# Performance work log

Hardware: AMD Instinct MI355X
Metric: run time of the kernel (lower is better)

## Reference

```python
import jax, jax.numpy as jnp
import numpy as np

S = 256          # spatial coordinate range per axis
B = 2            # batch size
R = S + 2        # packing radix (padded so +-1 kernel offsets stay in range)
C = 64           # feature channels


def _pack(xyz, b):
    """Collision-free integer packing of (x,y,z,batch) -> int64 key.
    Faithful stand-in for torchsparse F.sphash (an injective hash of 4D coords)."""
    xyz = xyz.astype(jnp.int64) + 1  # shift so offset -1 maps to >= 0
    b = b.astype(jnp.int64)
    return ((b * R + xyz[:, 0]) * R + xyz[:, 1]) * R + xyz[:, 2]


def _offsets():
    # get_kernel_offsets(3, stride=input_stride=1, dilation=1): odd kernel -> z-major order
    r = np.arange(-1, 2)
    return np.array([[x, y, z] for z in r for y in r for x in r], dtype=np.int32)  # [27, 3]


def setup_inputs() -> dict:
    rng = np.random.default_rng(0)
    N0 = 1_200_000
    xyz = rng.integers(0, S, size=(N0, 3))
    bat = rng.integers(0, B, size=(N0, 1))
    coords = np.unique(np.concatenate([xyz, bat], axis=1), axis=0).astype(np.int32)  # [N,4]
    # spdownsample(coords, stride=2): floor to stride grid, unique rows
    dc = coords.copy()
    dc[:, :3] = dc[:, :3] // 2 * 2
    down_coords = np.unique(dc, axis=0).astype(np.int32)  # [M,4]
    key = jax.random.key(0)
    feats = jax.random.normal(key, (coords.shape[0], C), dtype=jnp.float32)
    return {
        "feats": feats,
        "coords": jnp.asarray(coords),
        "down_coords": jnp.asarray(down_coords),
    }


def reference(feats, coords, down_coords):
    N = feats.shape[0]
    # references = sphash(coords); build sorted key table for hash queries
    refs = _pack(coords[:, :3], coords[:, 3])
    order = jnp.argsort(refs)
    refs_sorted = refs[order]
    neg = jnp.asarray(-jnp.inf, feats.dtype)
    out = jnp.full((down_coords.shape[0], feats.shape[1]), neg, feats.dtype)
    # queries = sphash(down_coords, offsets); results = sphashquery; voxel_scatter_max
    # (output row of each nbmap entry is the query row, so scatter-max reduces to a
    #  per-row running maximum over the 27 fixed kernel offsets)
    for off in _offsets():
        q = _pack(down_coords[:, :3] + jnp.asarray(off), down_coords[:, 3])
        pos = jnp.clip(jnp.searchsorted(refs_sorted, q), 0, N - 1)
        match = refs_sorted[pos] == q            # [M] valid-neighbor mask (result != -1)
        src = order[pos]                          # [M] input voxel index per query
        out = jnp.maximum(out, jnp.where(match[:, None], feats[src], neg))
    # rows with no neighbor (cannot happen for stride-2 floor downsample) -> 0
    return jnp.where(jnp.isinf(out), jnp.asarray(0.0, feats.dtype), out)
```

## Files before the change

### kernel.cpp

```cpp
#include <hip/hip_runtime.h>
#include <cstdint>
#include <cstddef>

#define RADIX 258
#define EMPTY_ENTRY 0xFFFFFFFFFFFFFFFFULL
#define MAP_DIM 128
#define MAP_SLOTS (2 * MAP_DIM * MAP_DIM * MAP_DIM)

typedef float f32x4 __attribute__((ext_vector_type(4)));


__global__ __launch_bounds__(256) void build_map_kernel(
    const int* __restrict__ down, int M, unsigned* __restrict__ map)
{
    int j = blockIdx.x * blockDim.x + threadIdx.x;
    if (j >= M) return;
    const int4 c = ((const int4*)down)[j];
    unsigned idx = (((unsigned)(c.w * MAP_DIM + (c.x >> 1)) * MAP_DIM)
                    + (unsigned)(c.y >> 1)) * MAP_DIM + (unsigned)(c.z >> 1);
    map[idx] = (unsigned)j;
}

__global__ __launch_bounds__(256) void scatter_kernel(
    const int* __restrict__ coords, int N,
    const unsigned* __restrict__ map,
    unsigned* __restrict__ cnt, unsigned* __restrict__ nbmap)
{
    int i = blockIdx.x * blockDim.x + threadIdx.x;
    if (i >= N) return;
    const int4 c = ((const int4*)coords)[i];
    int qx[2], qy[2], qz[2];
    int nx = 1, ny = 1, nz = 1;
    if (c.x & 1) { qx[0] = (c.x - 1) >> 1; if (c.x + 1 <= 254) qx[nx++] = (c.x + 1) >> 1; }
    else         { qx[0] = c.x >> 1; }
    if (c.y & 1) { qy[0] = (c.y - 1) >> 1; if (c.y + 1 <= 254) qy[ny++] = (c.y + 1) >> 1; }
    else         { qy[0] = c.y >> 1; }
    if (c.z & 1) { qz[0] = (c.z - 1) >> 1; if (c.z + 1 <= 254) qz[nz++] = (c.z + 1) >> 1; }
    else         { qz[0] = c.z >> 1; }
    unsigned bbase = (unsigned)(c.w * MAP_DIM);
    for (int ix = 0; ix < nx; ++ix) {
        unsigned xb = (bbase + (unsigned)qx[ix]) * MAP_DIM;
        for (int iy = 0; iy < ny; ++iy) {
            unsigned yb = (xb + (unsigned)qy[iy]) * MAP_DIM;
            for (int iz = 0; iz < nz; ++iz) {
                unsigned qi = map[yb + (unsigned)qz[iz]];
                if (qi != 0xFFFFFFFFu) {
                    unsigned pos = atomicAdd(&cnt[qi], 1u);
                    nbmap[(size_t)qi * 27 + pos] = (unsigned)i;
                }
            }
        }
    }
}

__global__ __launch_bounds__(256) void gather4_kernel(
    const float* __restrict__ feats,
    const unsigned* __restrict__ cnt,
    const unsigned* __restrict__ nbmap,
    float* __restrict__ out, int M, int nwg)
{
    int bid = blockIdx.x;
    int q = nwg >> 3, r = nwg & 7;
    int xcd = bid & 7, orig = bid >> 3;
    int swz = (xcd < r ? xcd * (q + 1) : r * (q + 1) + (xcd - r) * q) + orig;

    int lane = threadIdx.x & 63;
    int g    = lane >> 4;
    int j    = lane & 15;
    int wave = swz * 4 + (int)(threadIdx.x >> 6);
    int row  = wave * 4 + g;
    bool valid = row < M;

    int c = valid ? (int)cnt[row] : 0;
    const unsigned* nb = nbmap + (size_t)row * 27;
    int idxA = 0;
    if (valid && j < c) idxA = (int)nb[j];

    const f32x4* f4 = (const f32x4*)feats;
    int gb = g << 4;
    f32x4 acc = {-INFINITY, -INFINITY, -INFINITY, -INFINITY};
    for (int r4 = 0; r4 < c; r4 += 4) {
        int cm1 = c - 1;
        int h0 = min(r4,     cm1);
        int h1 = min(r4 + 1, cm1);
        int h2 = min(r4 + 2, cm1);
        int h3 = min(r4 + 3, cm1);
        int a0 = __shfl(idxA, gb + min(h0, 15));
        int a1 = __shfl(idxA, gb + min(h1, 15));
        int a2 = __shfl(idxA, gb + min(h2, 15));
        int a3 = __shfl(idxA, gb + min(h3, 15));
        int s0 = (h0 < 16) ? a0 : (int)nb[h0];
        int s1 = (h1 < 16) ? a1 : (int)nb[h1];
        int s2 = (h2 < 16) ? a2 : (int)nb[h2];
        int s3 = (h3 < 16) ? a3 : (int)nb[h3];
        f32x4 v0 = f4[(size_t)s0 * 16 + j];
        f32x4 v1 = f4[(size_t)s1 * 16 + j];
        f32x4 v2 = f4[(size_t)s2 * 16 + j];
        f32x4 v3 = f4[(size_t)s3 * 16 + j];
        acc.x = fmaxf(fmaxf(fmaxf(acc.x, v0.x), fmaxf(v1.x, v2.x)), v3.x);
        acc.y = fmaxf(fmaxf(fmaxf(acc.y, v0.y), fmaxf(v1.y, v2.y)), v3.y);
        acc.z = fmaxf(fmaxf(fmaxf(acc.z, v0.z), fmaxf(v1.z, v2.z)), v3.z);
        acc.w = fmaxf(fmaxf(fmaxf(acc.w, v0.w), fmaxf(v1.w, v2.w)), v3.w);
    }
    if (valid) {
        if (c == 0) acc = (f32x4){0.f, 0.f, 0.f, 0.f};
        __builtin_nontemporal_store(acc, (f32x4*)out + (size_t)row * 16 + j);
    }
}


__global__ __launch_bounds__(256) void build_hash_kernel(
    const int* __restrict__ coords, int N,
    unsigned long long* __restrict__ tab, unsigned tmask, int tshift)
{
    int i = blockIdx.x * blockDim.x + threadIdx.x;
    if (i >= N) return;
    int x = coords[i * 4 + 0];
    int y = coords[i * 4 + 1];
    int z = coords[i * 4 + 2];
    int b = coords[i * 4 + 3];
    unsigned key = ((unsigned)(b * RADIX + x + 1) * RADIX + (unsigned)(y + 1)) * RADIX
                   + (unsigned)(z + 1);
    unsigned long long entry = ((unsigned long long)key << 32) | (unsigned)i;
    unsigned slot = (key * 2654435761u) >> tshift;
    while (true) {
        unsigned long long prev = atomicCAS(&tab[slot], EMPTY_ENTRY, entry);
        if (prev == EMPTY_ENTRY) break;
        slot = (slot + 1) & tmask;
    }
}

__global__ __launch_bounds__(256) void pool_kernel(
    const float* __restrict__ feats,
    const int* __restrict__ down, int M,
    const unsigned long long* __restrict__ tab, unsigned tmask, int tshift,
    float* __restrict__ out)
{
    int wave = (int)((blockIdx.x * blockDim.x + threadIdx.x) >> 6);
    int lane = threadIdx.x & 63;
    if (wave >= M) return;

    const int* dc = down + (size_t)wave * 4;
    int dx = dc[0], dy = dc[1], dz = dc[2], db = dc[3];
    unsigned base = ((unsigned)(db * RADIX + dx + 1) * RADIX + (unsigned)(dy + 1)) * RADIX
                    + (unsigned)(dz + 1);

    int src = -1;
    if (lane < 27) {
        int ox = lane % 3 - 1;
        int oy = (lane / 3) % 3 - 1;
        int oz = lane / 9 - 1;
        int delta = ox * (RADIX * RADIX) + oy * RADIX + oz;
        unsigned key = (unsigned)((int)base + delta);
        unsigned slot = (key * 2654435761u) >> tshift;
        while (true) {
            unsigned long long e = tab[slot];
            if (e == EMPTY_ENTRY) break;
            if ((unsigned)(e >> 32) == key) { src = (int)(unsigned)e; break; }
            slot = (slot + 1) & tmask;
        }
    }
    unsigned long long mask = __ballot(src >= 0);
    float acc = -INFINITY;
    while (mask) {
        int bit = __ffsll(mask) - 1;
        int s = __shfl(src, bit);
        acc = fmaxf(acc, feats[(size_t)s * 64 + lane]);
        mask &= mask - 1;
    }
    out[(size_t)wave * 64 + lane] = isinf(acc) ? 0.0f : acc;
}


extern "C" void kernel_launch(void* const* d_in, const int* in_sizes, int n_in,
                              void* d_out, int out_size, void* d_ws, size_t ws_size,
                              hipStream_t stream)
{
    const float* feats  = (const float*)d_in[0];
    const int*   coords = (const int*)d_in[1];
    const int*   down   = (const int*)d_in[2];
    float*       out    = (float*)d_out;

    int N = in_sizes[1] / 4;
    int M = in_sizes[2] / 4;

    size_t map_bytes = (size_t)MAP_SLOTS * 4;
    size_t cnt_bytes = (size_t)M * 4;
    size_t nb_bytes  = (size_t)M * 27 * 4;
    size_t need = map_bytes + cnt_bytes + nb_bytes;

    if (ws_size >= need) {
        unsigned* map   = (unsigned*)d_ws;
        unsigned* cnt   = (unsigned*)((char*)d_ws + map_bytes);
        unsigned* nbmap = (unsigned*)((char*)d_ws + map_bytes + cnt_bytes);

        hipMemsetAsync(map, 0xFF, map_bytes, stream);
        hipMemsetAsync(cnt, 0x00, cnt_bytes, stream);

        build_map_kernel<<<(M + 255) / 256, 256, 0, stream>>>(down, M, map);
        scatter_kernel<<<(N + 255) / 256, 256, 0, stream>>>(coords, N, map, cnt, nbmap);

        int nwg = (M + 15) / 16;
        gather4_kernel<<<nwg, 256, 0, stream>>>(feats, cnt, nbmap, out, M, nwg);
    } else {
        int logT = 22;
        while (logT > 19 && ((size_t)8u << logT) > ws_size) logT--;
        unsigned T = 1u << logT;
        unsigned tmask = T - 1u;
        int tshift = 32 - logT;
        unsigned long long* tab = (unsigned long long*)d_ws;
        hipMemsetAsync(tab, 0xFF, (size_t)T * 8, stream);
        build_hash_kernel<<<(N + 255) / 256, 256, 0, stream>>>(coords, N, tab, tmask, tshift);
        pool_kernel<<<(M * 64 + 255) / 256, 256, 0, stream>>>(
            feats, down, M, tab, tmask, tshift, out);
    }
}
```

Before: 208.7 us.

## Interleave neighbor counts into padded nbmap rows and fuse clears into one kernel

The separate count array is removed. Each down-voxel's neighbor count now sits in the first word of a 32-word nbmap row, so the gather reads count and indices in one coalesced 64-byte load per 16-lane group. The two memsets are replaced by a single clear kernel that fills the map and zeroes each row's count word. The gather loop is also simplified to per-element predicated loads. The trade-off is a larger nbmap footprint, and the scatter atomics now land on padded rows.

Result: slower. 290.3 us (+39.1%).

```diff
diff --git a/kernel.cpp b/kernel.cpp
--- a/kernel.cpp
+++ b/kernel.cpp
@@ -6,9 +6,22 @@
 #define EMPTY_ENTRY 0xFFFFFFFFFFFFFFFFULL
 #define MAP_DIM 128
 #define MAP_SLOTS (2 * MAP_DIM * MAP_DIM * MAP_DIM)
+#define NB_STRIDE 32
 
 typedef float f32x4 __attribute__((ext_vector_type(4)));
 
+
+__global__ __launch_bounds__(256) void clear_kernel(
+    unsigned* __restrict__ map, unsigned* __restrict__ nbmap, int M)
+{
+    int t = blockIdx.x * blockDim.x + threadIdx.x;
+    const int mapVec = MAP_SLOTS / 4;
+    if (t < mapVec) {
+        ((uint4*)map)[t] = make_uint4(0xFFFFFFFFu, 0xFFFFFFFFu, 0xFFFFFFFFu, 0xFFFFFFFFu);
+    }
+    int u = t - mapVec;
+    if (u >= 0 && u < M) nbmap[(size_t)u * NB_STRIDE] = 0u;
+}
 
 __global__ __launch_bounds__(256) void build_map_kernel(
     const int* __restrict__ down, int M, unsigned* __restrict__ map)
@@ -24,7 +37,7 @@
 __global__ __launch_bounds__(256) void scatter_kernel(
     const int* __restrict__ coords, int N,
     const unsigned* __restrict__ map,
-    unsigned* __restrict__ cnt, unsigned* __restrict__ nbmap)
+    unsigned* __restrict__ nbmap)
 {
     int i = blockIdx.x * blockDim.x + threadIdx.x;
     if (i >= N) return;
@@ -45,17 +58,16 @@
             for (int iz = 0; iz < nz; ++iz) {
                 unsigned qi = map[yb + (unsigned)qz[iz]];
                 if (qi != 0xFFFFFFFFu) {
-                    unsigned pos = atomicAdd(&cnt[qi], 1u);
-                    nbmap[(size_t)qi * 27 + pos] = (unsigned)i;
+                    unsigned pos = atomicAdd(&nbmap[(size_t)qi * NB_STRIDE], 1u);
+                    nbmap[(size_t)qi * NB_STRIDE + 1 + pos] = (unsigned)i;
                 }
             }
         }
     }
 }
 
-__global__ __launch_bounds__(256) void gather4_kernel(
+__global__ __launch_bounds__(256) void gather_kernel(
     const float* __restrict__ feats,
-    const unsigned* __restrict__ cnt,
     const unsigned* __restrict__ nbmap,
     float* __restrict__ out, int M, int nwg)
 {
@@ -71,36 +83,27 @@
     int row  = wave * 4 + g;
     bool valid = row < M;
 
-    int c = valid ? (int)cnt[row] : 0;
-    const unsigned* nb = nbmap + (size_t)row * 27;
-    int idxA = 0;
-    if (valid && j < c) idxA = (int)nb[j];
+    unsigned w = 0;
+    if (valid) w = __builtin_nontemporal_load(&nbmap[(size_t)row * NB_STRIDE + j]);
+    int gb = g << 4;
+    int c = __shfl((int)w, gb);
 
     const f32x4* f4 = (const f32x4*)feats;
-    int gb = g << 4;
     f32x4 acc = {-INFINITY, -INFINITY, -INFINITY, -INFINITY};
     for (int r4 = 0; r4 < c; r4 += 4) {
-        int cm1 = c - 1;
-        int h0 = min(r4,     cm1);
-        int h1 = min(r4 + 1, cm1);
-        int h2 = min(r4 + 2, cm1);
-        int h3 = min(r4 + 3, cm1);
-        int a0 = __shfl(idxA, gb + min(h0, 15));
-        int a1 = __shfl(idxA, gb + min(h1, 15));
-        int a2 = __shfl(idxA, gb + min(h2, 15));
-        int a3 = __shfl(idxA, gb + min(h3, 15));
-        int s0 = (h0 < 16) ? a0 : (int)nb[h0];
-        int s1 = (h1 < 16) ? a1 : (int)nb[h1];
-        int s2 = (h2 < 16) ? a2 : (int)nb[h2];
-        int s3 = (h3 < 16) ? a3 : (int)nb[h3];
-        f32x4 v0 = f4[(size_t)s0 * 16 + j];
-        f32x4 v1 = f4[(size_t)s1 * 16 + j];
-        f32x4 v2 = f4[(size_t)s2 * 16 + j];
-        f32x4 v3 = f4[(size_t)s3 * 16 + j];
-        acc.x = fmaxf(fmaxf(fmaxf(acc.x, v0.x), fmaxf(v1.x, v2.x)), v3.x);
-        acc.y = fmaxf(fmaxf(fmaxf(acc.y, v0.y), fmaxf(v1.y, v2.y)), v3.y);
-        acc.z = fmaxf(fmaxf(fmaxf(acc.z, v0.z), fmaxf(v1.z, v2.z)), v3.z);
-        acc.w = fmaxf(fmaxf(fmaxf(acc.w, v0.w), fmaxf(v1.w, v2.w)), v3.w);
+#pragma unroll
+        for (int k = 0; k < 4; ++k) {
+            int h = r4 + k;
+            if (h < c) {
+                int s = (h < 15) ? __shfl((int)w, gb + 1 + h)
+                                 : (int)nbmap[(size_t)row * NB_STRIDE + 1 + h];
+                f32x4 v = f4[(size_t)s * 16 + j];
+                acc.x = fmaxf(acc.x, v.x);
+                acc.y = fmaxf(acc.y, v.y);
+                acc.z = fmaxf(acc.z, v.z);
+                acc.w = fmaxf(acc.w, v.w);
+            }
+        }
     }
     if (valid) {
         if (c == 0) acc = (f32x4){0.f, 0.f, 0.f, 0.f};
@@ -185,23 +188,20 @@
     int M = in_sizes[2] / 4;
 
     size_t map_bytes = (size_t)MAP_SLOTS * 4;
-    size_t cnt_bytes = (size_t)M * 4;
-    size_t nb_bytes  = (size_t)M * 27 * 4;
-    size_t need = map_bytes + cnt_bytes + nb_bytes;
+    size_t nb_bytes  = (size_t)((M + 15) & ~15) * NB_STRIDE * 4;
+    size_t need = map_bytes + nb_bytes;
 
     if (ws_size >= need) {
         unsigned* map   = (unsigned*)d_ws;
-        unsigned* cnt   = (unsigned*)((char*)d_ws + map_bytes);
-        unsigned* nbmap = (unsigned*)((char*)d_ws + map_bytes + cnt_bytes);
-
-        hipMemsetAsync(map, 0xFF, map_bytes, stream);
-        hipMemsetAsync(cnt, 0x00, cnt_bytes, stream);
-
+        unsigned* nbmap = (unsigned*)((char*)d_ws + map_bytes);
+
+        int clearThreads = MAP_SLOTS / 4 + M;
+        clear_kernel<<<(clearThreads + 255) / 256, 256, 0, stream>>>(map, nbmap, M);
         build_map_kernel<<<(M + 255) / 256, 256, 0, stream>>>(down, M, map);
-        scatter_kernel<<<(N + 255) / 256, 256, 0, stream>>>(coords, N, map, cnt, nbmap);
+        scatter_kernel<<<(N + 255) / 256, 256, 0, stream>>>(coords, N, map, nbmap);
 
         int nwg = (M + 15) / 16;
-        gather4_kernel<<<nwg, 256, 0, stream>>>(feats, cnt, nbmap, out, M, nwg);
+        gather_kernel<<<nwg, 256, 0, stream>>>(feats, nbmap, out, M, nwg);
     } else {
         int logT = 22;
         while (logT > 19 && ((size_t)8u << logT) > ws_size) logT--;
```
